# Performance work log

Hardware: AMD Instinct MI355X
Metric: run time of the kernel (lower is better)

## Reference

```python
import jax, jax.numpy as jnp
import numpy as np

N_A = 50000
N_B = 50000
E = 500000
HID = 128
NEG_SLOPE = 0.2
LN_EPS = 1e-5


def _ln(x, g, b):
    mu = jnp.mean(x, axis=-1, keepdims=True)
    var = jnp.mean((x - mu) ** 2, axis=-1, keepdims=True)
    return (x - mu) * jax.lax.rsqrt(var + LN_EPS) * g + b


def _gat(x_src, x_dst, src, dst, W, a_src, a_dst, bias, H, D, n_dst):
    # PyG GATConv (shared lin for src/dst, add_self_loops=False, eval mode)
    hs = (x_src @ W).reshape(-1, H, D)              # [N_src, H, D]
    hd = (x_dst @ W).reshape(-1, H, D)              # [N_dst, H, D]
    a_s = jnp.einsum('nhd,hd->nh', hs, a_src)       # per-node src score
    a_d = jnp.einsum('nhd,hd->nh', hd, a_dst)       # per-node dst score
    e = jax.nn.leaky_relu(a_s[src] + a_d[dst], NEG_SLOPE)   # [E, H]
    m = jax.ops.segment_max(e, dst, num_segments=n_dst)     # segment softmax
    m = jnp.where(jnp.isfinite(m), m, 0.0)
    ex = jnp.exp(e - m[dst])
    s = jax.ops.segment_sum(ex, dst, num_segments=n_dst)
    alpha = ex / (s[dst] + 1e-16)                   # [E, H]
    msg = hs[src] * alpha[:, :, None]               # [E, H, D]
    out = jax.ops.segment_sum(msg, dst, num_segments=n_dst) # [N_dst, H, D]
    return out.reshape(n_dst, H * D) + bias


def setup_inputs() -> dict:
    key = jax.random.key(0)
    ks = jax.random.split(key, 32)
    f32 = jnp.float32

    def rn(k, sh, s=0.05):
        return jax.random.normal(k, sh, dtype=f32) * s

    inp = {}
    inp['x_A'] = jax.random.normal(ks[0], (N_A, 128), dtype=f32)
    inp['x_B'] = jax.random.normal(ks[1], (N_B, 64), dtype=f32)
    inp['pWA'] = rn(ks[2], (128, HID)); inp['pbA'] = rn(ks[3], (HID,))
    inp['pWB'] = rn(ks[4], (64, HID)); inp['pbB'] = rn(ks[5], (HID,))
    inp['w0ab'] = rn(ks[6], (HID, HID)); inp['as0ab'] = rn(ks[7], (4, 32))
    inp['ad0ab'] = rn(ks[8], (4, 32)); inp['b0ab'] = rn(ks[9], (HID,))
    inp['w0ba'] = rn(ks[10], (HID, HID)); inp['as0ba'] = rn(ks[11], (4, 32))
    inp['ad0ba'] = rn(ks[12], (4, 32)); inp['b0ba'] = rn(ks[13], (HID,))
    inp['w1ab'] = rn(ks[14], (HID, HID)); inp['as1ab'] = rn(ks[15], (1, HID))
    inp['ad1ab'] = rn(ks[16], (1, HID)); inp['b1ab'] = rn(ks[17], (HID,))
    inp['w1ba'] = rn(ks[18], (HID, HID)); inp['as1ba'] = rn(ks[19], (1, HID))
    inp['ad1ba'] = rn(ks[20], (1, HID)); inp['b1ba'] = rn(ks[21], (HID,))
    for i, nm in enumerate(['0A', '0B', '1A', '1B']):
        inp['g' + nm] = jnp.ones((HID,), dtype=f32)
        inp['bn' + nm] = jnp.zeros((HID,), dtype=f32)
    inp['ei_AB'] = jax.random.randint(ks[22], (2, E), 0, N_B)  # src in A, dst in B
    inp['ei_BA'] = jax.random.randint(ks[23], (2, E), 0, N_A)  # src in B, dst in A
    return inp


def reference(x_A, x_B, pWA, pbA, pWB, pbB,
              w0ab, as0ab, ad0ab, b0ab, w0ba, as0ba, ad0ba, b0ba,
              w1ab, as1ab, ad1ab, b1ab, w1ba, as1ba, ad1ba, b1ba,
              g0A, bn0A, g0B, bn0B, g1A, bn1A, g1B, bn1B,
              ei_AB, ei_BA):
    # input projections (dropout is eval-mode no-op)
    hA = x_A @ pWA + pbA
    hB = x_B @ pWB + pbB
    # layer 0: heads=4, d_head=32, concat -> 128
    pA, pB = hA, hB
    nB = _gat(hA, hB, ei_AB[0], ei_AB[1], w0ab, as0ab, ad0ab, b0ab, 4, 32, N_B)
    nA = _gat(hB, hA, ei_BA[0], ei_BA[1], w0ba, as0ba, ad0ba, b0ba, 4, 32, N_A)
    hA = jax.nn.relu(_ln(nA, g0A, bn0A)) + pA
    hB = jax.nn.relu(_ln(nB, g0B, bn0B)) + pB
    # layer 1: heads=1, out=128
    pA, pB = hA, hB
    nB = _gat(hA, hB, ei_AB[0], ei_AB[1], w1ab, as1ab, ad1ab, b1ab, 1, HID, N_B)
    nA = _gat(hB, hA, ei_BA[0], ei_BA[1], w1ba, as1ba, ad1ba, b1ba, 1, HID, N_A)
    hA = jax.nn.relu(_ln(nA, g1A, bn1A)) + pA
    hB = jax.nn.relu(_ln(nB, g1B, bn1B)) + pB
    return hA, hB
```

## Files before the change

kernel.cpp:

```cpp
#include <hip/hip_runtime.h>
#include <hip/hip_bf16.h>

using bf16 = __hip_bfloat16;
using frag8 = __attribute__((ext_vector_type(8))) short;
using f32x4 = __attribute__((ext_vector_type(4))) float;

__device__ __forceinline__ short f2bf_bits(float f) {
  bf16 h = __float2bfloat16(f);
  short s; __builtin_memcpy(&s, &h, 2); return s;
}
__device__ __forceinline__ float bfbits2f(unsigned short u) {
  unsigned uu = (unsigned)u << 16; float f; __builtin_memcpy(&f, &uu, 4); return f;
}
__device__ __forceinline__ float wred_sum(float v) {
#pragma unroll
  for (int o = 32; o; o >>= 1) v += __shfl_xor(v, o);
  return v;
}

struct ConvJob { const void* src; void* dst; int n; int mode; int ksh; };
struct ConvJobs { ConvJob j[28]; };
struct WtJob { const void* wraw; const void* adraw; bf16* out; int H; };
struct WtJobs4 { WtJob j[4]; };

__global__ __launch_bounds__(256) void prep_k(
    const unsigned* __restrict__ xdet, int* __restrict__ flag,
    ConvJobs cjobs, int ncv, WtJobs4 wjobs,
    int* __restrict__ cntA, int nA, int* __restrict__ cntB, int nB)
{
  const int b = blockIdx.x, tid = threadIdx.x;
  if (b >= ncv + 4) {
    int i = (b - (ncv + 4)) * 256 + tid;
    if (i < nA) cntA[i] = 0;
    else if (i < nA + nB) cntB[i - nA] = 0;
    return;
  }
  __shared__ int sh[256];
  int c = 0;
  for (int i = tid; i < 4096; i += 256) {
    unsigned bb = (xdet[i] >> 8) & 0x7F;
    c += (bb >= 0x3B && bb <= 0x41) ? 1 : 0;
  }
  sh[tid] = c; __syncthreads();
  for (int off = 128; off; off >>= 1) { if (tid < off) sh[tid] += sh[tid + off]; __syncthreads(); }
  const int f = (sh[0] < 2048) ? 1 : 0;
  if (b == 0 && tid == 0) flag[0] = f;

  if (b < ncv) {
    ConvJob J = cjobs.j[b];
    const int Kt = 1 << J.ksh;
    for (int i = tid; i < J.n; i += 256) {
      int si = i;
      if (J.mode == 1) { int n = i >> J.ksh, k = i & (Kt - 1); si = k * 128 + n; }
      float v = f ? ((const float*)J.src)[si] : bfbits2f(((const unsigned short*)J.src)[si]);
      if (J.mode == 1) ((bf16*)J.dst)[i] = __float2bfloat16(v);
      else             ((float*)J.dst)[i] = v;
    }
  } else {
    WtJob J = wjobs.j[b - ncv];
    const int H = J.H, D = 128 / H;
    for (int idx = tid; idx < 16 * 128; idx += 256) {
      int h = idx >> 7, k = idx & 127;
      float s = 0.f;
      if (h < H) {
        for (int d = 0; d < D; d++) {
          int n = h * D + d;
          float wv = f ? ((const float*)J.wraw)[k * 128 + n]
                       : bfbits2f(((const unsigned short*)J.wraw)[k * 128 + n]);
          float av = f ? ((const float*)J.adraw)[n]
                       : bfbits2f(((const unsigned short*)J.adraw)[n]);
          s += wv * av;
        }
      }
      J.out[idx] = __float2bfloat16(s);
    }
  }
}

struct GemmJob {
  const void* Av; const bf16* WT; const float* bias; const float* avec;
  bf16* outFull; float* outScore; const int* flagp;
  const bf16* WT2; float* outScore2;
  int M, K, H, H2;
};
__device__ __forceinline__ void gemm_body(const GemmJob& J, int blk) {
  __shared__ __align__(16) bf16 Wt[128 * 136];
  __shared__ __align__(16) bf16 Wt2s[16 * 136];
  const int tid = threadIdx.x;
  const int K = J.K;
  const int isf32 = J.flagp ? J.flagp[0] : 0;
  const int stride = K + 8;
  const int ksh2 = (K == 128) ? 4 : 3;
  const int kunits = K >> 3;
  for (int u = tid; u < 128 * kunits; u += 256) {
    int n = u >> ksh2, kb = u & (kunits - 1);
    frag8 v = *(const frag8*)(J.WT + n * K + kb * 8);
    *(frag8*)(Wt + n * stride + kb * 8) = v;
  }
  if (J.WT2) {
    int n = tid >> 4, kb = tid & 15;
    *(frag8*)(Wt2s + n * 136 + kb * 8) = *(const frag8*)(J.WT2 + n * 128 + kb * 8);
  }
  __syncthreads();

  const int lane = tid & 63, wave = tid >> 6;
  const int quad = lane >> 4, c = lane & 15;
  const int mbase = blk * 64 + wave * 16;
  const int arow = mbase + c;
  const bool rowOK = arow < J.M;

  f32x4 acc[8];
#pragma unroll
  for (int t = 0; t < 8; t++) acc[t] = (f32x4){0.f, 0.f, 0.f, 0.f};
  f32x4 acc2 = (f32x4){0.f, 0.f, 0.f, 0.f};

  for (int ks = 0; ks < K; ks += 32) {
    frag8 af;
    const int k0 = ks + quad * 8;
    if (rowOK) {
      if (isf32) {
        const float4* ap = (const float4*)((const float*)J.Av + (size_t)arow * K + k0);
        float4 v0 = ap[0], v1 = ap[1];
        af[0] = f2bf_bits(v0.x); af[1] = f2bf_bits(v0.y);
        af[2] = f2bf_bits(v0.z); af[3] = f2bf_bits(v0.w);
        af[4] = f2bf_bits(v1.x); af[5] = f2bf_bits(v1.y);
        af[6] = f2bf_bits(v1.z); af[7] = f2bf_bits(v1.w);
      } else {
        af = *(const frag8*)((const bf16*)J.Av + (size_t)arow * K + k0);
      }
    } else {
#pragma unroll
      for (int j = 0; j < 8; j++) af[j] = 0;
    }
#pragma unroll
    for (int t = 0; t < 8; t++) {
      frag8 bfv = *(const frag8*)(Wt + (t * 16 + c) * stride + k0);
      acc[t] = __builtin_amdgcn_mfma_f32_16x16x32_bf16(af, bfv, acc[t], 0, 0, 0);
    }
    if (J.WT2) {
      frag8 b2 = *(const frag8*)(Wt2s + c * 136 + k0);
      acc2 = __builtin_amdgcn_mfma_f32_16x16x32_bf16(af, b2, acc2, 0, 0, 0);
    }
  }

  if (J.outFull) {
#pragma unroll
    for (int t = 0; t < 8; t++) {
#pragma unroll
      for (int r = 0; r < 4; r++) {
        int orow = mbase + quad * 4 + r;
        if (orow < J.M) {
          float v = acc[t][r];
          if (J.bias) v += J.bias[t * 16 + c];
          J.outFull[(size_t)orow * 128 + t * 16 + c] = __float2bfloat16(v);
        }
      }
    }
  }
  if (J.outScore) {
    const int H = J.H;
    const int TPH = 8 / H;
    for (int hh = 0; hh < H; hh++) {
#pragma unroll
      for (int r = 0; r < 4; r++) {
        float p = 0.f;
        for (int tt = 0; tt < TPH; tt++) {
          int t = hh * TPH + tt;
          p += acc[t][r] * J.avec[t * 16 + c];
        }
#pragma unroll
        for (int off = 1; off < 16; off <<= 1) p += __shfl_xor(p, off);
        int orow = mbase + quad * 4 + r;
        if (c == 0 && orow < J.M) J.outScore[(size_t)orow * H + hh] = p;
      }
    }
  }
  if (J.outScore2) {
#pragma unroll
    for (int r = 0; r < 4; r++) {
      int orow = mbase + quad * 4 + r;
      if (c < J.H2 && orow < J.M) J.outScore2[(size_t)orow * J.H2 + c] = acc2[r];
    }
  }
}

__global__ __launch_bounds__(256) void histgemm_k(
    GemmJob ja, GemmJob jb, int gsplit,
    const int* __restrict__ dAB, const int* __restrict__ dBA, int E, int geh,
    int* __restrict__ cntB, int* __restrict__ cntA)
{
  const int b = blockIdx.x;
  if (b < 2 * geh) {
    if (b < geh) { int i = b * 256 + threadIdx.x; if (i < E) atomicAdd(&cntB[dAB[i]], 1); }
    else { int i = (b - geh) * 256 + threadIdx.x; if (i < E) atomicAdd(&cntA[dBA[i]], 1); }
    return;
  }
  const int gb = b - 2 * geh;
  if (gb < gsplit) gemm_body(ja, gb);
  else             gemm_body(jb, gb - gsplit);
}

__device__ __forceinline__ void blocksum_body(const int* cnt, int N, int* bsum, int blk) {
  __shared__ int sh[256];
  const int tid = threadIdx.x;
  const int beg = blk * 1024;
  const int end = (beg + 1024 < N) ? beg + 1024 : N;
  int loc = 0;
  for (int i = beg + tid; i < end; i += 256) loc += cnt[i];
  sh[tid] = loc; __syncthreads();
  for (int off = 128; off; off >>= 1) { if (tid < off) sh[tid] += sh[tid + off]; __syncthreads(); }
  if (tid == 0) bsum[blk] = sh[0];
}
__global__ __launch_bounds__(256) void blocksum2_k(
    const int* __restrict__ cntB, int NB, int* __restrict__ bsumB, int nbB,
    const int* __restrict__ cntA, int NA, int* __restrict__ bsumA)
{
  int b = blockIdx.x;
  if (b < nbB) blocksum_body(cntB, NB, bsumB, b);
  else         blocksum_body(cntA, NA, bsumA, b - nbB);
}
__device__ __forceinline__ void writerp_body(const int* cnt, int N, const int* bsum,
                                             int* rp, int* cur, int blk) {
  __shared__ int sh[256];
  const int tid = threadIdx.x;
  int offacc = 0;
  for (int i = tid; i < blk; i += 256) offacc += bsum[i];
  sh[tid] = offacc; __syncthreads();
  for (int off = 128; off; off >>= 1) { if (tid < off) sh[tid] += sh[tid + off]; __syncthreads(); }
  const int base = sh[0];
  __syncthreads();

  const int idx0 = blk * 1024 + tid * 4;
  int c[4]; int loc = 0;
#pragma unroll
  for (int j = 0; j < 4; j++) {
    int i = idx0 + j;
    c[j] = (i < N) ? cnt[i] : 0;
    loc += c[j];
  }
  sh[tid] = loc; __syncthreads();
  for (int off = 1; off < 256; off <<= 1) {
    int x = sh[tid];
    int o = (tid >= off) ? sh[tid - off] : 0;
    __syncthreads();
    sh[tid] = x + o;
    __syncthreads();
  }
  int run = base + ((tid == 0) ? 0 : sh[tid - 1]);
#pragma unroll
  for (int j = 0; j < 4; j++) {
    int i = idx0 + j;
    if (i < N) { rp[i] = run; cur[i] = run; }
    run += c[j];
  }
  if (idx0 <= N - 1 && N - 1 < idx0 + 4) rp[N] = run;
}
__global__ __launch_bounds__(256) void writerp2_k(
    const int* __restrict__ cntB, int NB, const int* __restrict__ bsumB,
    int* __restrict__ rpAB, int* __restrict__ curB, int nbB,
    const int* __restrict__ cntA, int NA, const int* __restrict__ bsumA,
    int* __restrict__ rpBA, int* __restrict__ curA)
{
  int b = blockIdx.x;
  if (b < nbB) writerp_body(cntB, NB, bsumB, rpAB, curB, b);
  else         writerp_body(cntA, NA, bsumA, rpBA, curA, b - nbB);
}

__global__ __launch_bounds__(256) void gemm2_k(GemmJob ja, GemmJob jb, int split) {
  if (blockIdx.x < split) gemm_body(ja, blockIdx.x);
  else                    gemm_body(jb, blockIdx.x - split);
}

__global__ __launch_bounds__(256) void scattgemm_k(
    GemmJob ja, GemmJob jb, int gsplit, int gtot,
    const int* __restrict__ sAB, const int* __restrict__ dAB,
    const int* __restrict__ sBA, const int* __restrict__ dBA, int E,
    int* __restrict__ curB, int* __restrict__ slAB,
    int* __restrict__ curA, int* __restrict__ slBA, int NB, int NA)
{
  int b = blockIdx.x;
  if (b < gtot) {
    if (b < gsplit) gemm_body(ja, b);
    else            gemm_body(jb, b - gsplit);
    return;
  }
  b -= gtot;
  const int g = b & 7;
  const int sidx = b >> 3;
  const int loB = (int)((long long)NB * g >> 3), hiB = (int)((long long)NB * (g + 1) >> 3);
  const int loA = (int)((long long)NA * g >> 3), hiA = (int)((long long)NA * (g + 1) >> 3);
  const int b0 = sidx * 2048;
#pragma unroll
  for (int j = 0; j < 8; j++) {
    int i = b0 + j * 256 + threadIdx.x;
    if (i < 2 * E) {
      bool ab = i < E;
      int k = ab ? i : i - E;
      int d = ab ? dAB[k] : dBA[k];
      int lo = ab ? loB : loA, hi = ab ? hiB : hiA;
      if (d >= lo && d < hi) {
        int sv = ab ? sAB[k] : sBA[k];
        int pos = atomicAdd((ab ? curB : curA) + d, 1);
        (ab ? slAB : slBA)[pos] = sv;
      }
    }
  }
}

struct AggJob {
  const int* rp; const int* srcl; const float* as_; const float* ad_;
  const bf16* hs; const float* bias; const float* gamma; const float* beta;
  const bf16* resid; bf16* outBf; void* outFinal; const int* flagp;
  int nodeBase, N;
};

template<int H, bool FINAL>
__global__ __launch_bounds__(256) void agg_k(AggJob JA, AggJob JB, int split) {
  const bool first = blockIdx.x < split;
  const AggJob J = first ? JA : JB;
  const int blk = first ? blockIdx.x : blockIdx.x - split;

  __shared__ int   s_src[4][64];
  __shared__ float s_p[4][64 * H];
  const int tid = threadIdx.x;
  const int wave = tid >> 6, lane = tid & 63;
  const int n = blk * 4 + wave;
  if (n >= J.N) return;

  const int beg = J.rp[n], end = J.rp[n + 1];
  const int qe = lane >> 4;
  const int ql = lane & 15;
  const int myh = (H == 4) ? (ql >> 2) : 0;

  float4 adv;
  if (H == 4) adv = *(const float4*)(J.ad_ + (size_t)n * 4);
  else        adv.x = J.ad_[n];

  float a0 = 0.f, a1 = 0.f, a2 = 0.f, a3 = 0.f;
  float a4 = 0.f, a5 = 0.f, a6 = 0.f, a7 = 0.f;
  float dacc = 0.f;
  const int* srcp = J.srcl;
  const float* asp = J.as_;
  const bf16* hsp = J.hs;

  for (int base = beg; base < end; base += 64) {
    const int cn = (end - base < 64) ? end - base : 64;
    if (lane < cn) {
      int s = srcp[base + lane];
      s_src[wave][lane] = s;
      if (H == 4) {
        float4 a = *(const float4*)(asp + (size_t)s * 4);
        float4 o; float v;
        v = a.x + adv.x; v = v > 0.f ? v : 0.2f * v; o.x = __expf(v);
        v = a.y + adv.y; v = v > 0.f ? v : 0.2f * v; o.y = __expf(v);
        v = a.z + adv.z; v = v > 0.f ? v : 0.2f * v; o.z = __expf(v);
        v = a.w + adv.w; v = v > 0.f ? v : 0.2f * v; o.w = __expf(v);
        *(float4*)&s_p[wave][lane * 4] = o;
      } else {
        float v = asp[s] + adv.x;
        v = v > 0.f ? v : 0.2f * v;
        s_p[wave][lane] = __expf(v);
      }
    }
    __builtin_amdgcn_wave_barrier();
#pragma unroll 4
    for (int e = 0; e < cn; e += 4) {
      const int eidx = e + qe;
      const bool val = eidx < cn;
      const int ei = val ? eidx : cn - 1;
      const int s = s_src[wave][ei];
      const float p = val ? s_p[wave][ei * H + myh] : 0.f;
      const uint4 u = *(const uint4*)(hsp + (size_t)s * 128 + ql * 8);
      dacc += p;
      a0 += p * bfbits2f((unsigned short)(u.x & 0xFFFF));
      a1 += p * bfbits2f((unsigned short)(u.x >> 16));
      a2 += p * bfbits2f((unsigned short)(u.y & 0xFFFF));
      a3 += p * bfbits2f((unsigned short)(u.y >> 16));
      a4 += p * bfbits2f((unsigned short)(u.z & 0xFFFF));
      a5 += p * bfbits2f((unsigned short)(u.z >> 16));
      a6 += p * bfbits2f((unsigned short)(u.w & 0xFFFF));
      a7 += p * bfbits2f((unsigned short)(u.w >> 16));
    }
    __builtin_amdgcn_wave_barrier();
  }

#pragma unroll
  for (int o = 16; o <= 32; o <<= 1) {
    a0 += __shfl_xor(a0, o); a1 += __shfl_xor(a1, o);
    a2 += __shfl_xor(a2, o); a3 += __shfl_xor(a3, o);
    a4 += __shfl_xor(a4, o); a5 += __shfl_xor(a5, o);
    a6 += __shfl_xor(a6, o); a7 += __shfl_xor(a7, o);
    dacc += __shfl_xor(dacc, o);
  }
  const float inv = 1.f / (dacc + 1e-16f);

  const float4 bi0 = *(const float4*)(J.bias + ql * 8);
  const float4 bi1 = *(const float4*)(J.bias + ql * 8 + 4);
  float y0 = a0 * inv + bi0.x, y1 = a1 * inv + bi0.y;
  float y2 = a2 * inv + bi0.z, y3 = a3 * inv + bi0.w;
  float y4 = a4 * inv + bi1.x, y5 = a5 * inv + bi1.y;
  float y6 = a6 * inv + bi1.z, y7 = a7 * inv + bi1.w;
  float tsum = wred_sum(y0 + y1 + y2 + y3 + y4 + y5 + y6 + y7);
  float tsq  = wred_sum(y0*y0 + y1*y1 + y2*y2 + y3*y3 + y4*y4 + y5*y5 + y6*y6 + y7*y7);
  float mu = tsum * 0.001953125f;
  float var = tsq * 0.001953125f - mu * mu;
  float rs = rsqrtf(var + 1e-5f);
  const float4 ga0 = *(const float4*)(J.gamma + ql * 8);
  const float4 ga1 = *(const float4*)(J.gamma + ql * 8 + 4);
  const float4 be0 = *(const float4*)(J.beta + ql * 8);
  const float4 be1 = *(const float4*)(J.beta + ql * 8 + 4);
  float z0 = (y0 - mu) * rs * ga0.x + be0.x;
  float z1 = (y1 - mu) * rs * ga0.y + be0.y;
  float z2 = (y2 - mu) * rs * ga0.z + be0.z;
  float z3 = (y3 - mu) * rs * ga0.w + be0.w;
  float z4 = (y4 - mu) * rs * ga1.x + be1.x;
  float z5 = (y5 - mu) * rs * ga1.y + be1.y;
  float z6 = (y6 - mu) * rs * ga1.z + be1.z;
  float z7 = (y7 - mu) * rs * ga1.w + be1.w;
  const uint4 ru = *(const uint4*)(J.resid + (size_t)n * 128 + ql * 8);
  z0 = fmaxf(z0, 0.f) + bfbits2f((unsigned short)(ru.x & 0xFFFF));
  z1 = fmaxf(z1, 0.f) + bfbits2f((unsigned short)(ru.x >> 16));
  z2 = fmaxf(z2, 0.f) + bfbits2f((unsigned short)(ru.y & 0xFFFF));
  z3 = fmaxf(z3, 0.f) + bfbits2f((unsigned short)(ru.y >> 16));
  z4 = fmaxf(z4, 0.f) + bfbits2f((unsigned short)(ru.z & 0xFFFF));
  z5 = fmaxf(z5, 0.f) + bfbits2f((unsigned short)(ru.z >> 16));
  z6 = fmaxf(z6, 0.f) + bfbits2f((unsigned short)(ru.w & 0xFFFF));
  z7 = fmaxf(z7, 0.f) + bfbits2f((unsigned short)(ru.w >> 16));

  if (qe == 0) {
    if constexpr (FINAL) {
      if (J.flagp[0]) {
        float* op = (float*)J.outFinal + (size_t)(J.nodeBase + n) * 128 + ql * 8;
        *(float4*)op = make_float4(z0, z1, z2, z3);
        *(float4*)(op + 4) = make_float4(z4, z5, z6, z7);
      } else {
        uint4 pk;
        pk.x = (unsigned)(unsigned short)f2bf_bits(z0) | ((unsigned)(unsigned short)f2bf_bits(z1) << 16);
        pk.y = (unsigned)(unsigned short)f2bf_bits(z2) | ((unsigned)(unsigned short)f2bf_bits(z3) << 16);
        pk.z = (unsigned)(unsigned short)f2bf_bits(z4) | ((unsigned)(unsigned short)f2bf_bits(z5) << 16);
        pk.w = (unsigned)(unsigned short)f2bf_bits(z6) | ((unsigned)(unsigned short)f2bf_bits(z7) << 16);
        *(uint4*)((bf16*)J.outFinal + (size_t)(J.nodeBase + n) * 128 + ql * 8) = pk;
      }
    } else {
      uint4 pk;
      pk.x = (unsigned)(unsigned short)f2bf_bits(z0) | ((unsigned)(unsigned short)f2bf_bits(z1) << 16);
      pk.y = (unsigned)(unsigned short)f2bf_bits(z2) | ((unsigned)(unsigned short)f2bf_bits(z3) << 16);
      pk.z = (unsigned)(unsigned short)f2bf_bits(z4) | ((unsigned)(unsigned short)f2bf_bits(z5) << 16);
      pk.w = (unsigned)(unsigned short)f2bf_bits(z6) | ((unsigned)(unsigned short)f2bf_bits(z7) << 16);
      *(uint4*)(J.outBf + (size_t)n * 128 + ql * 8) = pk;
    }
  }
}

extern "C" void kernel_launch(void* const* d_in, const int* in_sizes, int n_in,
                              void* d_out, int out_size, void* d_ws, size_t ws_size,
                              hipStream_t stream)
{
  const int NA = in_sizes[0] / 128;
  const int NB = in_sizes[1] / 64;
  const int E  = in_sizes[30] / 2;
  const int* eiAB = (const int*)d_in[30];
  const int* eiBA = (const int*)d_in[31];
  const int* srcAB = eiAB;  const int* dstAB = eiAB + E;
  const int* srcBA = eiBA;  const int* dstBA = eiBA + E;

  char* w = (char*)d_ws;
  size_t used = 0;
  auto alloc = [&](size_t bytes) {
    char* p = w + used;
    used += (bytes + 255) & ~size_t(255);
    return (void*)p;
  };
  int*  flag  = (int*)alloc(256);
  bf16* WcA   = (bf16*)alloc(16384 * 2);
  bf16* WcB   = (bf16*)alloc(8192 * 2);
  bf16* Wc0ab = (bf16*)alloc(16384 * 2);
  bf16* Wc0ba = (bf16*)alloc(16384 * 2);
  bf16* Wc1ab = (bf16*)alloc(16384 * 2);
  bf16* Wc1ba = (bf16*)alloc(16384 * 2);
  bf16* Wt0ab = (bf16*)alloc(16 * 128 * 2);
  bf16* Wt0ba = (bf16*)alloc(16 * 128 * 2);
  bf16* Wt1ab = (bf16*)alloc(16 * 128 * 2);
  bf16* Wt1ba = (bf16*)alloc(16 * 128 * 2);
  float* vec  = (float*)alloc(22 * 128 * 4);
  bf16* hA    = (bf16*)alloc((size_t)NA * 128 * 2);
  bf16* hB    = (bf16*)alloc((size_t)NB * 128 * 2);
  bf16* hsAB  = (bf16*)alloc((size_t)NA * 128 * 2);
  bf16* hsBA  = (bf16*)alloc((size_t)NB * 128 * 2);
  float* asAB = (float*)alloc((size_t)NA * 4 * 4);
  float* adAB = (float*)alloc((size_t)NB * 4 * 4);
  float* asBA = (float*)alloc((size_t)NB * 4 * 4);
  float* adBA = (float*)alloc((size_t)NA * 4 * 4);
  int* rpAB = (int*)alloc((size_t)(NB + 1) * 4);
  int* slAB = (int*)alloc((size_t)E * 4);
  int* rpBA = (int*)alloc((size_t)(NA + 1) * 4);
  int* slBA = (int*)alloc((size_t)E * 4);
  int* cntA = (int*)alloc((size_t)NA * 4);
  int* curA = (int*)alloc((size_t)NA * 4);
  int* cntB = (int*)alloc((size_t)NB * 4);
  int* curB = (int*)alloc((size_t)NB * 4);
  int* bsumA = (int*)alloc(256 * 4);
  int* bsumB = (int*)alloc(256 * 4);
  if (used > ws_size) return;

  auto V = [&](int i) { return vec + 128 * i; };

  ConvJobs jobs{};
  int nj = 0;
  auto addT = [&](const void* s, void* d, int K) {
    int ksh = (K == 128) ? 7 : 6;
    jobs.j[nj++] = ConvJob{s, d, 128 * K, 1, ksh};
  };
  auto addV = [&](const void* s, void* d) { jobs.j[nj++] = ConvJob{s, d, 128, 0, 7}; };
  addT(d_in[2], WcA, 128);
  addT(d_in[4], WcB, 64);
  addT(d_in[6], Wc0ab, 128);
  addT(d_in[10], Wc0ba, 128);
  addT(d_in[14], Wc1ab, 128);
  addT(d_in[18], Wc1ba, 128);
  const int vsrc[22] = {3, 5, 7, 8, 9, 11, 12, 13, 15, 16, 17, 19, 20, 21, 22, 23, 24, 25, 26, 27, 28, 29};
  for (int i = 0; i < 22; i++) addV(d_in[vsrc[i]], V(i));

  WtJobs4 wj{};
  wj.j[0] = WtJob{d_in[6],  d_in[8],  Wt0ab, 4};
  wj.j[1] = WtJob{d_in[10], d_in[12], Wt0ba, 4};
  wj.j[2] = WtJob{d_in[14], d_in[16], Wt1ab, 1};
  wj.j[3] = WtJob{d_in[18], d_in[20], Wt1ba, 1};

  const int nz = (NA + NB + 255) / 256;
  prep_k<<<nj + 4 + nz, 256, 0, stream>>>((const unsigned*)d_in[0], flag, jobs, nj, wj,
                                          cntA, NA, cntB, NB);

  const int geh = (E + 255) / 256;
  const int gA = (NA + 63) / 64, gB = (NB + 63) / 64;
  const int aA = (NA + 3) / 4, aB = (NB + 3) / 4;
  const int nbB = (NB + 1023) / 1024, nbA = (NA + 1023) / 1024;

  {
    GemmJob ja{d_in[0], WcA, V(0), nullptr, hA, nullptr, flag, nullptr, nullptr, NA, 128, 1, 0};
    GemmJob jb{d_in[1], WcB, V(1), nullptr, hB, nullptr, flag, nullptr, nullptr, NB, 64, 1, 0};
    histgemm_k<<<2 * geh + gA + gB, 256, 0, stream>>>(ja, jb, gA, dstAB, dstBA, E, geh,
                                                      cntB, cntA);
  }
  blocksum2_k<<<nbB + nbA, 256, 0, stream>>>(cntB, NB, bsumB, nbB, cntA, NA, bsumA);
  writerp2_k<<<nbB + nbA, 256, 0, stream>>>(cntB, NB, bsumB, rpAB, curB, nbB,
                                            cntA, NA, bsumA, rpBA, curA);
  {
    GemmJob ja{hA, Wc0ab, nullptr, V(2), hsAB, asAB, nullptr, Wt0ba, adBA, NA, 128, 4, 4};
    GemmJob jb{hB, Wc0ba, nullptr, V(5), hsBA, asBA, nullptr, Wt0ab, adAB, NB, 128, 4, 4};
    const int gtot = gA + gB;
    const int nsl = (2 * E + 2047) / 2048;
    scattgemm_k<<<gtot + 8 * nsl, 256, 0, stream>>>(ja, jb, gA, gtot,
                                                    srcAB, dstAB, srcBA, dstBA, E,
                                                    curB, slAB, curA, slBA, NB, NA);
  }
  {
    AggJob ja{rpAB, slAB, asAB, adAB, hsAB, V(4), V(16), V(17), hB, hB, nullptr, nullptr, 0, NB};
    AggJob jb{rpBA, slBA, asBA, adBA, hsBA, V(7), V(14), V(15), hA, hA, nullptr, nullptr, 0, NA};
    agg_k<4, false><<<aB + aA, 256, 0, stream>>>(ja, jb, aB);
  }
  {
    GemmJob ja{hA, Wc1ab, nullptr, V(8),  hsAB, asAB, nullptr, Wt1ba, adBA, NA, 128, 1, 1};
    GemmJob jb{hB, Wc1ba, nullptr, V(11), hsBA, asBA, nullptr, Wt1ab, adAB, NB, 128, 1, 1};
    gemm2_k<<<gA + gB, 256, 0, stream>>>(ja, jb, gA);
  }
  {
    AggJob ja{rpAB, slAB, asAB, adAB, hsAB, V(10), V(20), V(21), hB, nullptr, d_out, flag, NA, NB};
    AggJob jb{rpBA, slBA, asBA, adBA, hsBA, V(13), V(18), V(19), hA, nullptr, d_out, flag, 0, NA};
    agg_k<1, true><<<aB + aA, 256, 0, stream>>>(ja, jb, aB);
  }
}
```

Measured before the change: 467.4 us.

## Co-schedule layer-0 GEMM with row-pointer write and split off edge scatter

```diff
diff --git a/kernel.cpp b/kernel.cpp
--- a/kernel.cpp
+++ b/kernel.cpp
@@ -219,6 +219,7 @@
   if (b < nbB) blocksum_body(cntB, NB, bsumB, b);
   else         blocksum_body(cntA, NA, bsumA, b - nbB);
 }
+
 __device__ __forceinline__ void writerp_body(const int* cnt, int N, const int* bsum,
                                              int* rp, int* cur, int blk) {
   __shared__ int sh[256];
@@ -255,15 +256,22 @@
   }
   if (idx0 <= N - 1 && N - 1 < idx0 + 4) rp[N] = run;
 }
-__global__ __launch_bounds__(256) void writerp2_k(
+__global__ __launch_bounds__(256) void wrpgemm_k(
+    GemmJob ja, GemmJob jb, int gsplit,
     const int* __restrict__ cntB, int NB, const int* __restrict__ bsumB,
     int* __restrict__ rpAB, int* __restrict__ curB, int nbB,
     const int* __restrict__ cntA, int NA, const int* __restrict__ bsumA,
-    int* __restrict__ rpBA, int* __restrict__ curA)
+    int* __restrict__ rpBA, int* __restrict__ curA, int nbA)
 {
-  int b = blockIdx.x;
-  if (b < nbB) writerp_body(cntB, NB, bsumB, rpAB, curB, b);
-  else         writerp_body(cntA, NA, bsumA, rpBA, curA, b - nbB);
+  const int b = blockIdx.x;
+  if (b < nbB + nbA) {
+    if (b < nbB) writerp_body(cntB, NB, bsumB, rpAB, curB, b);
+    else         writerp_body(cntA, NA, bsumA, rpBA, curA, b - nbB);
+    return;
+  }
+  const int gb = b - (nbB + nbA);
+  if (gb < gsplit) gemm_body(ja, gb);
+  else             gemm_body(jb, gb - gsplit);
 }
 
 __global__ __launch_bounds__(256) void gemm2_k(GemmJob ja, GemmJob jb, int split) {
@@ -271,22 +279,14 @@
   else                    gemm_body(jb, blockIdx.x - split);
 }
 
-__global__ __launch_bounds__(256) void scattgemm_k(
-    GemmJob ja, GemmJob jb, int gsplit, int gtot,
+__global__ __launch_bounds__(256) void scatter8_k(
     const int* __restrict__ sAB, const int* __restrict__ dAB,
     const int* __restrict__ sBA, const int* __restrict__ dBA, int E,
     int* __restrict__ curB, int* __restrict__ slAB,
     int* __restrict__ curA, int* __restrict__ slBA, int NB, int NA)
 {
-  int b = blockIdx.x;
-  if (b < gtot) {
-    if (b < gsplit) gemm_body(ja, b);
-    else            gemm_body(jb, b - gsplit);
-    return;
-  }
-  b -= gtot;
-  const int g = b & 7;
-  const int sidx = b >> 3;
+  const int g = blockIdx.x & 7;
+  const int sidx = blockIdx.x >> 3;
   const int loB = (int)((long long)NB * g >> 3), hiB = (int)((long long)NB * (g + 1) >> 3);
   const int loA = (int)((long long)NA * g >> 3), hiA = (int)((long long)NA * (g + 1) >> 3);
   const int b0 = sidx * 2048;
@@ -363,7 +363,7 @@
       }
     }
     __builtin_amdgcn_wave_barrier();
-#pragma unroll 4
+#pragma unroll 8
     for (int e = 0; e < cn; e += 4) {
       const int eidx = e + qe;
       const bool val = eidx < cn;
@@ -543,16 +543,17 @@
                                                       cntB, cntA);
   }
   blocksum2_k<<<nbB + nbA, 256, 0, stream>>>(cntB, NB, bsumB, nbB, cntA, NA, bsumA);
-  writerp2_k<<<nbB + nbA, 256, 0, stream>>>(cntB, NB, bsumB, rpAB, curB, nbB,
-                                            cntA, NA, bsumA, rpBA, curA);
   {
     GemmJob ja{hA, Wc0ab, nullptr, V(2), hsAB, asAB, nullptr, Wt0ba, adBA, NA, 128, 4, 4};
     GemmJob jb{hB, Wc0ba, nullptr, V(5), hsBA, asBA, nullptr, Wt0ab, adAB, NB, 128, 4, 4};
-    const int gtot = gA + gB;
+    wrpgemm_k<<<nbB + nbA + gA + gB, 256, 0, stream>>>(ja, jb, gA,
+                                                       cntB, NB, bsumB, rpAB, curB, nbB,
+                                                       cntA, NA, bsumA, rpBA, curA, nbA);
+  }
+  {
     const int nsl = (2 * E + 2047) / 2048;
-    scattgemm_k<<<gtot + 8 * nsl, 256, 0, stream>>>(ja, jb, gA, gtot,
-                                                    srcAB, dstAB, srcBA, dstBA, E,
-                                                    curB, slAB, curA, slBA, NB, NA);
+    scatter8_k<<<8 * nsl, 256, 0, stream>>>(srcAB, dstAB, srcBA, dstBA, E,
+                                            curB, slAB, curA, slBA, NB, NA);
   }
   {
     AggJob ja{rpAB, slAB, asAB, adAB, hsAB, V(4), V(16), V(17), hB, hB, nullptr, nullptr, 0, NB};
```

Result: slower. 502.3 us (+7.5%).

## Replace per-node CSR build with two-pass bucketed radix sort of edges

Applied to the files above, without the earlier changes.

```diff
diff --git a/kernel.cpp b/kernel.cpp
--- a/kernel.cpp
+++ b/kernel.cpp
@@ -26,13 +26,26 @@
 __global__ __launch_bounds__(256) void prep_k(
     const unsigned* __restrict__ xdet, int* __restrict__ flag,
     ConvJobs cjobs, int ncv, WtJobs4 wjobs,
-    int* __restrict__ cntA, int nA, int* __restrict__ cntB, int nB)
+    const int* __restrict__ dAB, const int* __restrict__ dBA, int E, int nch,
+    int* __restrict__ gcntB, int* __restrict__ gcntA, int wshB, int wshA)
 {
   const int b = blockIdx.x, tid = threadIdx.x;
   if (b >= ncv + 4) {
-    int i = (b - (ncv + 4)) * 256 + tid;
-    if (i < nA) cntA[i] = 0;
-    else if (i < nA + nB) cntB[i - nA] = 0;
+    __shared__ int h[256];
+    h[tid] = 0; __syncthreads();
+    const int cb = b - (ncv + 4);
+    const bool ab = cb < nch;
+    const int* dp = ab ? dAB : dBA;
+    int* gc = ab ? gcntB : gcntA;
+    const int wsh = ab ? wshB : wshA;
+    const int base = (ab ? cb : cb - nch) * 2048;
+#pragma unroll
+    for (int j = 0; j < 8; j++) {
+      int i = base + j * 256 + tid;
+      if (i < E) atomicAdd(&h[dp[i] >> wsh], 1);
+    }
+    __syncthreads();
+    if (h[tid]) atomicAdd(&gc[tid], h[tid]);
     return;
   }
   __shared__ int sh[256];
@@ -184,99 +197,14 @@
   }
 }
 
-__global__ __launch_bounds__(256) void histgemm_k(
-    GemmJob ja, GemmJob jb, int gsplit,
-    const int* __restrict__ dAB, const int* __restrict__ dBA, int E, int geh,
-    int* __restrict__ cntB, int* __restrict__ cntA)
-{
-  const int b = blockIdx.x;
-  if (b < 2 * geh) {
-    if (b < geh) { int i = b * 256 + threadIdx.x; if (i < E) atomicAdd(&cntB[dAB[i]], 1); }
-    else { int i = (b - geh) * 256 + threadIdx.x; if (i < E) atomicAdd(&cntA[dBA[i]], 1); }
-    return;
-  }
-  const int gb = b - 2 * geh;
-  if (gb < gsplit) gemm_body(ja, gb);
-  else             gemm_body(jb, gb - gsplit);
-}
-
-__device__ __forceinline__ void blocksum_body(const int* cnt, int N, int* bsum, int blk) {
-  __shared__ int sh[256];
-  const int tid = threadIdx.x;
-  const int beg = blk * 1024;
-  const int end = (beg + 1024 < N) ? beg + 1024 : N;
-  int loc = 0;
-  for (int i = beg + tid; i < end; i += 256) loc += cnt[i];
-  sh[tid] = loc; __syncthreads();
-  for (int off = 128; off; off >>= 1) { if (tid < off) sh[tid] += sh[tid + off]; __syncthreads(); }
-  if (tid == 0) bsum[blk] = sh[0];
-}
-__global__ __launch_bounds__(256) void blocksum2_k(
-    const int* __restrict__ cntB, int NB, int* __restrict__ bsumB, int nbB,
-    const int* __restrict__ cntA, int NA, int* __restrict__ bsumA)
-{
-  int b = blockIdx.x;
-  if (b < nbB) blocksum_body(cntB, NB, bsumB, b);
-  else         blocksum_body(cntA, NA, bsumA, b - nbB);
-}
-__device__ __forceinline__ void writerp_body(const int* cnt, int N, const int* bsum,
-                                             int* rp, int* cur, int blk) {
-  __shared__ int sh[256];
-  const int tid = threadIdx.x;
-  int offacc = 0;
-  for (int i = tid; i < blk; i += 256) offacc += bsum[i];
-  sh[tid] = offacc; __syncthreads();
-  for (int off = 128; off; off >>= 1) { if (tid < off) sh[tid] += sh[tid + off]; __syncthreads(); }
-  const int base = sh[0];
-  __syncthreads();
-
-  const int idx0 = blk * 1024 + tid * 4;
-  int c[4]; int loc = 0;
-#pragma unroll
-  for (int j = 0; j < 4; j++) {
-    int i = idx0 + j;
-    c[j] = (i < N) ? cnt[i] : 0;
-    loc += c[j];
-  }
-  sh[tid] = loc; __syncthreads();
-  for (int off = 1; off < 256; off <<= 1) {
-    int x = sh[tid];
-    int o = (tid >= off) ? sh[tid - off] : 0;
-    __syncthreads();
-    sh[tid] = x + o;
-    __syncthreads();
-  }
-  int run = base + ((tid == 0) ? 0 : sh[tid - 1]);
-#pragma unroll
-  for (int j = 0; j < 4; j++) {
-    int i = idx0 + j;
-    if (i < N) { rp[i] = run; cur[i] = run; }
-    run += c[j];
-  }
-  if (idx0 <= N - 1 && N - 1 < idx0 + 4) rp[N] = run;
-}
-__global__ __launch_bounds__(256) void writerp2_k(
-    const int* __restrict__ cntB, int NB, const int* __restrict__ bsumB,
-    int* __restrict__ rpAB, int* __restrict__ curB, int nbB,
-    const int* __restrict__ cntA, int NA, const int* __restrict__ bsumA,
-    int* __restrict__ rpBA, int* __restrict__ curA)
-{
-  int b = blockIdx.x;
-  if (b < nbB) writerp_body(cntB, NB, bsumB, rpAB, curB, b);
-  else         writerp_body(cntA, NA, bsumA, rpBA, curA, b - nbB);
-}
-
-__global__ __launch_bounds__(256) void gemm2_k(GemmJob ja, GemmJob jb, int split) {
-  if (blockIdx.x < split) gemm_body(ja, blockIdx.x);
-  else                    gemm_body(jb, blockIdx.x - split);
-}
-
-__global__ __launch_bounds__(256) void scattgemm_k(
+__global__ __launch_bounds__(256) void bsctgemm_k(
     GemmJob ja, GemmJob jb, int gsplit, int gtot,
     const int* __restrict__ sAB, const int* __restrict__ dAB,
-    const int* __restrict__ sBA, const int* __restrict__ dBA, int E,
-    int* __restrict__ curB, int* __restrict__ slAB,
-    int* __restrict__ curA, int* __restrict__ slBA, int NB, int NA)
+    const int* __restrict__ sBA, const int* __restrict__ dBA, int E, int nch,
+    const int* __restrict__ gcntB, int* __restrict__ resvB,
+    unsigned* __restrict__ bkeyAB, int nbB,
+    const int* __restrict__ gcntA, int* __restrict__ resvA,
+    unsigned* __restrict__ bkeyBA, int nbA, int wshB, int wshA)
 {
   int b = blockIdx.x;
   if (b < gtot) {
@@ -285,26 +213,121 @@
     return;
   }
   b -= gtot;
-  const int g = b & 7;
-  const int sidx = b >> 3;
-  const int loB = (int)((long long)NB * g >> 3), hiB = (int)((long long)NB * (g + 1) >> 3);
-  const int loA = (int)((long long)NA * g >> 3), hiA = (int)((long long)NA * (g + 1) >> 3);
-  const int b0 = sidx * 2048;
+  const bool ab = b < nch;
+  const int* sp = ab ? sAB : sBA;
+  const int* dp = ab ? dAB : dBA;
+  const int* gc = ab ? gcntB : gcntA;
+  int* rv = ab ? resvB : resvA;
+  unsigned* bk = ab ? bkeyAB : bkeyBA;
+  const int nbuck = ab ? nbB : nbA;
+  const int wsh = ab ? wshB : wshA;
+  const int tid = threadIdx.x;
+  const int cbase = (ab ? b : b - nch) * 2048;
+
+  __shared__ int hh[256], ro[256], gb[256], tmp[256];
+  hh[tid] = 0; __syncthreads();
+  int sv[8], dv[8];
 #pragma unroll
   for (int j = 0; j < 8; j++) {
-    int i = b0 + j * 256 + threadIdx.x;
-    if (i < 2 * E) {
-      bool ab = i < E;
-      int k = ab ? i : i - E;
-      int d = ab ? dAB[k] : dBA[k];
-      int lo = ab ? loB : loA, hi = ab ? hiB : hiA;
-      if (d >= lo && d < hi) {
-        int sv = ab ? sAB[k] : sBA[k];
-        int pos = atomicAdd((ab ? curB : curA) + d, 1);
-        (ab ? slAB : slBA)[pos] = sv;
-      }
-    }
-  }
+    int i = cbase + j * 256 + tid;
+    if (i < E) { sv[j] = sp[i]; dv[j] = dp[i]; atomicAdd(&hh[dv[j] >> wsh], 1); }
+    else dv[j] = -1;
+  }
+  __syncthreads();
+  int g = (tid < nbuck) ? gc[tid] : 0;
+  tmp[tid] = g; __syncthreads();
+  for (int off = 1; off < 256; off <<= 1) {
+    int x = tmp[tid]; int o = (tid >= off) ? tmp[tid - off] : 0;
+    __syncthreads(); tmp[tid] = x + o; __syncthreads();
+  }
+  gb[tid] = tmp[tid] - g;
+  int c = hh[tid];
+  ro[tid] = c ? atomicAdd(&rv[tid], c) : 0;
+  __syncthreads();
+  hh[tid] = 0; __syncthreads();
+#pragma unroll
+  for (int j = 0; j < 8; j++) {
+    if (dv[j] >= 0) {
+      int v = dv[j] >> wsh;
+      int r = atomicAdd(&hh[v], 1);
+      bk[gb[v] + ro[v] + r] = ((unsigned)dv[j] << 16) | (unsigned)sv[j];
+    }
+  }
+}
+
+__global__ __launch_bounds__(256) void fsctgemm_k(
+    GemmJob ja, GemmJob jb, int gsplit, int gtot,
+    const unsigned* __restrict__ bkeyAB, const int* __restrict__ gcntB,
+    int* __restrict__ rpAB, int* __restrict__ slAB, int NB, int nbB, int wshB,
+    const unsigned* __restrict__ bkeyBA, const int* __restrict__ gcntA,
+    int* __restrict__ rpBA, int* __restrict__ slBA, int NA, int nbA, int wshA,
+    int E)
+{
+  int b = blockIdx.x;
+  if (b < gtot) {
+    if (b < gsplit) gemm_body(ja, b);
+    else            gemm_body(jb, b - gsplit);
+    return;
+  }
+  b -= gtot;
+  const bool ab = b < nbB;
+  const unsigned* bk = ab ? bkeyAB : bkeyBA;
+  const int* gc = ab ? gcntB : gcntA;
+  int* rp = ab ? rpAB : rpBA;
+  int* sl = ab ? slAB : slBA;
+  const int N = ab ? NB : NA;
+  const int nbuck = ab ? nbB : nbA;
+  const int wsh = ab ? wshB : wshA;
+  const int bkt = ab ? b : b - nbB;
+  const int tid = threadIdx.x;
+
+  __shared__ int tmp[256];
+  __shared__ int h[2048];
+  int g = (tid < nbuck) ? gc[tid] : 0;
+  tmp[tid] = g; __syncthreads();
+  for (int off = 1; off < 256; off <<= 1) {
+    int x = tmp[tid]; int o = (tid >= off) ? tmp[tid - off] : 0;
+    __syncthreads(); tmp[tid] = x + o; __syncthreads();
+  }
+  const int cnt  = gc[bkt];
+  const int base = tmp[bkt] - cnt;
+  const int win = 1 << wsh;
+  const int d0 = bkt << wsh;
+  for (int v = tid; v < win; v += 256) h[v] = 0;
+  __syncthreads();
+  for (int i = tid; i < cnt; i += 256) {
+    int v = (int)(bk[base + i] >> 16) - d0;
+    atomicAdd(&h[v], 1);
+  }
+  __syncthreads();
+  const int seg = win >> 8;
+  int loc = 0;
+  for (int j = 0; j < seg; j++) loc += h[tid * seg + j];
+  tmp[tid] = loc; __syncthreads();
+  for (int off = 1; off < 256; off <<= 1) {
+    int x = tmp[tid]; int o = (tid >= off) ? tmp[tid - off] : 0;
+    __syncthreads(); tmp[tid] = x + o; __syncthreads();
+  }
+  int run = tmp[tid] - loc;
+  for (int j = 0; j < seg; j++) { int c = h[tid * seg + j]; h[tid * seg + j] = run; run += c; }
+  __syncthreads();
+  for (int v = tid; v < win; v += 256) {
+    int d = d0 + v;
+    if (d < N) rp[d] = base + h[v];
+  }
+  if (bkt == 0 && tid == 0) rp[N] = E;
+  __syncthreads();
+  for (int i = tid; i < cnt; i += 256) {
+    unsigned k = bk[base + i];
+    int v = (int)(k >> 16) - d0;
+    int r = atomicAdd(&h[v], 1);
+    sl[base + r] = (int)(k & 0xFFFFu);
+  }
+}
+
+__global__ __launch_bounds__(256) void gemm2_k(GemmJob ja, GemmJob jb, int split) {
+  if (blockIdx.x < split) gemm_body(ja, blockIdx.x);
+  else                    gemm_body(jb, blockIdx.x - split);
 }
 
 struct AggJob {
@@ -464,6 +487,11 @@
   const int* srcAB = eiAB;  const int* dstAB = eiAB + E;
   const int* srcBA = eiBA;  const int* dstBA = eiBA + E;
 
+  int wshB = 8; while (((NB - 1) >> wshB) >= 256) wshB++;
+  int wshA = 8; while (((NA - 1) >> wshA) >= 256) wshA++;
+  const int nbB = ((NB - 1) >> wshB) + 1;
+  const int nbA = ((NA - 1) >> wshA) + 1;
+
   char* w = (char*)d_ws;
   size_t used = 0;
   auto alloc = [&](size_t bytes) {
@@ -472,6 +500,9 @@
     return (void*)p;
   };
   int*  flag  = (int*)alloc(256);
+  int*  zarr  = (int*)alloc(4096);
+  int* gcntB = zarr;       int* gcntA = zarr + 256;
+  int* resvB = zarr + 512; int* resvA = zarr + 768;
   bf16* WcA   = (bf16*)alloc(16384 * 2);
   bf16* WcB   = (bf16*)alloc(8192 * 2);
   bf16* Wc0ab = (bf16*)alloc(16384 * 2);
@@ -495,12 +526,8 @@
   int* slAB = (int*)alloc((size_t)E * 4);
   int* rpBA = (int*)alloc((size_t)(NA + 1) * 4);
   int* slBA = (int*)alloc((size_t)E * 4);
-  int* cntA = (int*)alloc((size_t)NA * 4);
-  int* curA = (int*)alloc((size_t)NA * 4);
-  int* cntB = (int*)alloc((size_t)NB * 4);
-  int* curB = (int*)alloc((size_t)NB * 4);
-  int* bsumA = (int*)alloc(256 * 4);
-  int* bsumB = (int*)alloc(256 * 4);
+  unsigned* bkeyAB = (unsigned*)alloc((size_t)E * 4);
+  unsigned* bkeyBA = (unsigned*)alloc((size_t)E * 4);
   if (used > ws_size) return;
 
   auto V = [&](int i) { return vec + 128 * i; };
@@ -527,32 +554,28 @@
   wj.j[2] = WtJob{d_in[14], d_in[16], Wt1ab, 1};
   wj.j[3] = WtJob{d_in[18], d_in[20], Wt1ba, 1};
 
-  const int nz = (NA + NB + 255) / 256;
-  prep_k<<<nj + 4 + nz, 256, 0, stream>>>((const unsigned*)d_in[0], flag, jobs, nj, wj,
-                                          cntA, NA, cntB, NB);
-
-  const int geh = (E + 255) / 256;
+  const int nch = (E + 2047) / 2048;
   const int gA = (NA + 63) / 64, gB = (NB + 63) / 64;
   const int aA = (NA + 3) / 4, aB = (NB + 3) / 4;
-  const int nbB = (NB + 1023) / 1024, nbA = (NA + 1023) / 1024;
-
+  const int gtot = gA + gB;
+
+  hipMemsetAsync(zarr, 0, 4096, stream);
+  prep_k<<<nj + 4 + 2 * nch, 256, 0, stream>>>((const unsigned*)d_in[0], flag, jobs, nj, wj,
+                                               dstAB, dstBA, E, nch, gcntB, gcntA, wshB, wshA);
   {
     GemmJob ja{d_in[0], WcA, V(0), nullptr, hA, nullptr, flag, nullptr, nullptr, NA, 128, 1, 0};
     GemmJob jb{d_in[1], WcB, V(1), nullptr, hB, nullptr, flag, nullptr, nullptr, NB, 64, 1, 0};
-    histgemm_k<<<2 * geh + gA + gB, 256, 0, stream>>>(ja, jb, gA, dstAB, dstBA, E, geh,
-                                                      cntB, cntA);
-  }
-  blocksum2_k<<<nbB + nbA, 256, 0, stream>>>(cntB, NB, bsumB, nbB, cntA, NA, bsumA);
-  writerp2_k<<<nbB + nbA, 256, 0, stream>>>(cntB, NB, bsumB, rpAB, curB, nbB,
-                                            cntA, NA, bsumA, rpBA, curA);
+    bsctgemm_k<<<gtot + 2 * nch, 256, 0, stream>>>(ja, jb, gA, gtot,
+                                                   srcAB, dstAB, srcBA, dstBA, E, nch,
+                                                   gcntB, resvB, bkeyAB, nbB,
+                                                   gcntA, resvA, bkeyBA, nbA, wshB, wshA);
+  }
   {
     GemmJob ja{hA, Wc0ab, nullptr, V(2), hsAB, asAB, nullptr, Wt0ba, adBA, NA, 128, 4, 4};
     GemmJob jb{hB, Wc0ba, nullptr, V(5), hsBA, asBA, nullptr, Wt0ab, adAB, NB, 128, 4, 4};
-    const int gtot = gA + gB;
-    const int nsl = (2 * E + 2047) / 2048;
-    scattgemm_k<<<gtot + 8 * nsl, 256, 0, stream>>>(ja, jb, gA, gtot,
-                                                    srcAB, dstAB, srcBA, dstBA, E,
-                                                    curB, slAB, curA, slBA, NB, NA);
+    fsctgemm_k<<<gtot + nbB + nbA, 256, 0, stream>>>(ja, jb, gA, gtot,
+                                                     bkeyAB, gcntB, rpAB, slAB, NB, nbB, wshB,
+                                                     bkeyBA, gcntA, rpBA, slBA, NA, nbA, wshA, E);
   }
   {
     AggJob ja{rpAB, slAB, asAB, adAB, hsAB, V(4), V(16), V(17), hB, hB, nullptr, nullptr, 0, NB};
@@ -562,7 +585,7 @@
   {
     GemmJob ja{hA, Wc1ab, nullptr, V(8),  hsAB, asAB, nullptr, Wt1ba, adBA, NA, 128, 1, 1};
     GemmJob jb{hB, Wc1ba, nullptr, V(11), hsBA, asBA, nullptr, Wt1ab, adAB, NB, 128, 1, 1};
-    gemm2_k<<<gA + gB, 256, 0, stream>>>(ja, jb, gA);
+    gemm2_k<<<gtot, 256, 0, stream>>>(ja, jb, gA);
   }
   {
     AggJob ja{rpAB, slAB, asAB, adAB, hsAB, V(10), V(20), V(21), hB, nullptr, d_out, flag, NA, NB};
```

After: 409.1 us. 12.5% less time.
